# Performance work log

Hardware: AMD Instinct MI355X
Metric: run time of the kernel (lower is better)

## Reference

```python
import jax, jax.numpy as jnp
import numpy as np

B, T, H, W = 1024, 10, 32, 32
D = H * W          # MoE token dim = image_width**2
HID = 2 * D        # MoE expert hidden size
E, K = 4, 1        # num_experts, top_k
N_MOE = 5          # transform, add, quad, cubic, fourth


def setup_inputs() -> dict:
    key = jax.random.key(0)
    ks = jax.random.split(key, 6)
    s = 0.02
    return {
        "input": jax.random.normal(ks[0], (B, T, 1, H, W), jnp.float32),
        "conv1_w": jax.random.normal(ks[1], (10, 1, 3, 3, 3), jnp.float32) * s,
        "conv1_b": jnp.zeros((10,), jnp.float32),
        "conv2_w": jax.random.normal(ks[2], (1, 10, T, 3, 3), jnp.float32) * s,
        "conv2_b": jnp.zeros((1,), jnp.float32),
        "w_gate": jax.random.normal(ks[3], (N_MOE, D, E), jnp.float32) * s,
        "w1": jax.random.normal(ks[4], (N_MOE, E, D, HID), jnp.float32) * s,
        "b1": jnp.zeros((N_MOE, E, HID), jnp.float32),
        "w2": jax.random.normal(ks[5], (N_MOE, E, HID, D), jnp.float32) * s,
        "b2": jnp.zeros((N_MOE, E, D), jnp.float32),
    }


def _conv3d(x, w, b, pad):
    y = jax.lax.conv_general_dilated(
        x, w, (1, 1, 1), pad, dimension_numbers=("NCDHW", "OIDHW", "NCDHW"))
    return y + b[None, :, None, None, None]


def _cv_squared(x):
    eps = 1e-10
    return jnp.var(x, ddof=1) / (jnp.mean(x) ** 2 + eps)


def _moe(tok, wg, w1, b1, w2, b2):
    # tok: (B, D). Eval-mode noisy-top-k gating (clean logits, no noise).
    logits = tok @ wg                                   # (B, E)
    top_vals, top_idx = jax.lax.top_k(logits, K)
    top_g = jax.nn.softmax(top_vals, axis=1)            # k=1 -> gate == 1.0
    gates = jnp.zeros_like(logits).at[
        jnp.arange(tok.shape[0])[:, None], top_idx].set(top_g)
    # dense all-expert MLP (E=4 is small), combined by sparse gates
    h = jax.nn.relu(jnp.einsum("bd,edh->beh", tok, w1) + b1)
    y = jnp.einsum("beh,ehd->bed", h, w2) + b2
    out = jnp.einsum("be,bed->bd", gates, y)
    importance = gates.sum(0)
    load = (gates > 0).astype(tok.dtype).sum(0)
    loss = (_cv_squared(importance) + _cv_squared(load)) * 1e-2
    return out, loss


def reference(input, conv1_w, conv1_b, conv2_w, conv2_b, w_gate, w1, b1, w2, b2):
    x = jnp.transpose(input, (0, 2, 1, 3, 4))           # (B,1,T,H,W)
    x = jax.nn.relu(_conv3d(x, conv1_w, conv1_b, [(1, 1), (1, 1), (1, 1)]))
    x = jax.nn.relu(_conv3d(x, conv2_w, conv2_b, [(0, 0), (1, 1), (1, 1)]))  # (B,1,1,H,W)
    tok = x.reshape(x.shape[0], -1)                     # (B, D)
    outs, losses = jax.vmap(_moe, in_axes=(None, 0, 0, 0, 0, 0))(
        tok, w_gate, w1, b1, w2, b2)                    # (5,B,D), (5,)
    f = outs.reshape(N_MOE, -1, 1, 1, H, W)             # each broadcasts over T
    transform, add, quad, cubic, fourth = f[0], f[1], f[2], f[3], f[4]
    i2 = input * input
    poly = (i2 * i2 * fourth + i2 * input * cubic + i2 * quad
            + input * transform + add)
    out = jax.nn.sigmoid(poly)                          # encoder/decoder = identity
    return out, jnp.sum(losses)
```

## Files before the change

### kernel.cpp

```cpp
#include <hip/hip_runtime.h>
#include <hip/hip_bf16.h>


typedef __bf16 bf16x8 __attribute__((ext_vector_type(8)));
typedef __bf16 bf16x4 __attribute__((ext_vector_type(4)));
typedef __bf16 bf16x2 __attribute__((ext_vector_type(2)));
typedef float f32x4 __attribute__((ext_vector_type(4)));

#define NMOE 5
#define NEXP 4

__global__ __launch_bounds__(256, 3) void conv_tok_kernel(
    const float* __restrict__ input, const float* __restrict__ c1w,
    const float* __restrict__ c1b, const float* __restrict__ c2w,
    const float* __restrict__ c2b, float* __restrict__ tok_f32,
    __bf16* __restrict__ tok_bf16)
{
    __shared__ float in_s[10][34][34];
    __shared__ float P[34][34];
    const int b = blockIdx.x, tid = threadIdx.x;

    float* ls = &in_s[0][0][0];
    for (int i = tid; i < 10 * 34 * 34; i += 256) ls[i] = 0.f;
    for (int i = tid; i < 34 * 34; i += 256) (&P[0][0])[i] = 0.f;
    __syncthreads();

    const float* ip = input + (size_t)b * 10240;
    for (int i = tid; i < 2560; i += 256) {
        int t = i >> 8, rem = i & 255;
        int h = rem >> 3, w4 = rem & 7;
        float4 v = ((const float4*)ip)[i];
        float* dst = &in_s[t][h + 1][w4 * 4 + 1];
        dst[0] = v.x; dst[1] = v.y; dst[2] = v.z; dst[3] = v.w;
    }
    __syncthreads();

    const int wcol = tid & 31;
    const int r0 = (tid >> 5) * 4;
    const float c2bias = c2b[0];
    float tk0 = c2bias, tk1 = c2bias, tk2 = c2bias, tk3 = c2bias;

    for (int c = 0; c < 10; ++c) {
        float w1l[27];
        #pragma unroll
        for (int i = 0; i < 27; ++i) w1l[i] = c1w[c * 27 + i];
        const float c1bias = c1b[c];

        float a0[10], a1[10], a2[10], a3[10];
        #pragma unroll
        for (int t = 0; t < 10; ++t) {
            a0[t] = c1bias; a1[t] = c1bias; a2[t] = c1bias; a3[t] = c1bias;
        }

        #pragma unroll
        for (int ts = 0; ts < 10; ++ts) {
            float p0[3], p1[3], p2[3], p3[3], p4[3], p5[3];
            #pragma unroll
            for (int dw = 0; dw < 3; ++dw) {
                p0[dw] = in_s[ts][r0 + 0][wcol + dw];
                p1[dw] = in_s[ts][r0 + 1][wcol + dw];
                p2[dw] = in_s[ts][r0 + 2][wcol + dw];
                p3[dw] = in_s[ts][r0 + 3][wcol + dw];
                p4[dw] = in_s[ts][r0 + 4][wcol + dw];
                p5[dw] = in_s[ts][r0 + 5][wcol + dw];
            }
            #pragma unroll
            for (int dt = 0; dt < 3; ++dt) {
                const int t = ts - dt + 1;
                if (t < 0 || t > 9) continue;
                #pragma unroll
                for (int dw = 0; dw < 3; ++dw) {
                    float u0 = w1l[dt * 9 + 0 + dw];
                    float u1 = w1l[dt * 9 + 3 + dw];
                    float u2 = w1l[dt * 9 + 6 + dw];
                    a0[t] += u0 * p0[dw] + u1 * p1[dw] + u2 * p2[dw];
                    a1[t] += u0 * p1[dw] + u1 * p2[dw] + u2 * p3[dw];
                    a2[t] += u0 * p2[dw] + u1 * p3[dw] + u2 * p4[dw];
                    a3[t] += u0 * p3[dw] + u1 * p4[dw] + u2 * p5[dw];
                }
            }
            if (ts >= 1) {
                const int td = ts - 1;
                __syncthreads();
                P[r0 + 1][wcol + 1] = fmaxf(a0[td], 0.f);
                P[r0 + 2][wcol + 1] = fmaxf(a1[td], 0.f);
                P[r0 + 3][wcol + 1] = fmaxf(a2[td], 0.f);
                P[r0 + 4][wcol + 1] = fmaxf(a3[td], 0.f);
                __syncthreads();
                const int wb = (c * 10 + td) * 9;
                #pragma unroll
                for (int dw = 0; dw < 3; ++dw) {
                    float q0 = P[r0 + 0][wcol + dw];
                    float q1 = P[r0 + 1][wcol + dw];
                    float q2 = P[r0 + 2][wcol + dw];
                    float q3 = P[r0 + 3][wcol + dw];
                    float q4 = P[r0 + 4][wcol + dw];
                    float q5 = P[r0 + 5][wcol + dw];
                    float u0 = c2w[wb + 0 + dw];
                    float u1 = c2w[wb + 3 + dw];
                    float u2 = c2w[wb + 6 + dw];
                    tk0 += u0 * q0 + u1 * q1 + u2 * q2;
                    tk1 += u0 * q1 + u1 * q2 + u2 * q3;
                    tk2 += u0 * q2 + u1 * q3 + u2 * q4;
                    tk3 += u0 * q3 + u1 * q4 + u2 * q5;
                }
            }
        }
        {
            __syncthreads();
            P[r0 + 1][wcol + 1] = fmaxf(a0[9], 0.f);
            P[r0 + 2][wcol + 1] = fmaxf(a1[9], 0.f);
            P[r0 + 3][wcol + 1] = fmaxf(a2[9], 0.f);
            P[r0 + 4][wcol + 1] = fmaxf(a3[9], 0.f);
            __syncthreads();
            const int wb = (c * 10 + 9) * 9;
            #pragma unroll
            for (int dw = 0; dw < 3; ++dw) {
                float q0 = P[r0 + 0][wcol + dw];
                float q1 = P[r0 + 1][wcol + dw];
                float q2 = P[r0 + 2][wcol + dw];
                float q3 = P[r0 + 3][wcol + dw];
                float q4 = P[r0 + 4][wcol + dw];
                float q5 = P[r0 + 5][wcol + dw];
                float u0 = c2w[wb + 0 + dw];
                float u1 = c2w[wb + 3 + dw];
                float u2 = c2w[wb + 6 + dw];
                tk0 += u0 * q0 + u1 * q1 + u2 * q2;
                tk1 += u0 * q1 + u1 * q2 + u2 * q3;
                tk2 += u0 * q2 + u1 * q3 + u2 * q4;
                tk3 += u0 * q3 + u1 * q4 + u2 * q5;
            }
        }
    }
    float o0 = fmaxf(tk0, 0.f), o1 = fmaxf(tk1, 0.f);
    float o2 = fmaxf(tk2, 0.f), o3 = fmaxf(tk3, 0.f);
    size_t base = (size_t)b * 1024 + (size_t)r0 * 32 + wcol;
    tok_f32[base] = o0; tok_f32[base + 32] = o1;
    tok_f32[base + 64] = o2; tok_f32[base + 96] = o3;
    tok_bf16[base] = (__bf16)o0; tok_bf16[base + 32] = (__bf16)o1;
    tok_bf16[base + 64] = (__bf16)o2; tok_bf16[base + 96] = (__bf16)o3;
}

__global__ __launch_bounds__(256) void gating_kernel(
    const float* __restrict__ tok, const float* __restrict__ w_gate,
    int* __restrict__ expert_id, int* __restrict__ counts)
{
    int gw = blockIdx.x * 4 + (threadIdx.x >> 6);
    int l = threadIdx.x & 63;
    int n = gw >> 10, b = gw & 1023;
    const float* trow = tok + (size_t)b * 1024;
    const float* wg = w_gate + (size_t)n * 4096;
    float a0 = 0.f, a1 = 0.f, a2 = 0.f, a3 = 0.f;
    #pragma unroll
    for (int i = 0; i < 16; ++i) {
        int d = i * 64 + l;
        float tv = trow[d];
        float4 g4 = *(const float4*)(wg + d * 4);
        a0 += tv * g4.x; a1 += tv * g4.y; a2 += tv * g4.z; a3 += tv * g4.w;
    }
    #pragma unroll
    for (int off = 32; off >= 1; off >>= 1) {
        a0 += __shfl_xor(a0, off);
        a1 += __shfl_xor(a1, off);
        a2 += __shfl_xor(a2, off);
        a3 += __shfl_xor(a3, off);
    }
    if (l == 0) {
        int e = 0; float best = a0;
        if (a1 > best) { best = a1; e = 1; }
        if (a2 > best) { best = a2; e = 2; }
        if (a3 > best) { best = a3; e = 3; }
        expert_id[n * 1024 + b] = e;
        atomicAdd(&counts[n * 4 + e], 1);
    }
}

__global__ __launch_bounds__(1024) void scatter_kernel(
    const int* __restrict__ expert_id, const int* __restrict__ counts,
    int* __restrict__ row_base, int* __restrict__ rows)
{
    __shared__ int cur[4];
    int n = blockIdx.x, tid = threadIdx.x;
    if (tid == 0) {
        int c0 = counts[n * 4 + 0], c1 = counts[n * 4 + 1], c2 = counts[n * 4 + 2];
        cur[0] = 0; cur[1] = c0; cur[2] = c0 + c1; cur[3] = c0 + c1 + c2;
        row_base[n * 4 + 0] = cur[0]; row_base[n * 4 + 1] = cur[1];
        row_base[n * 4 + 2] = cur[2]; row_base[n * 4 + 3] = cur[3];
    }
    __syncthreads();
    int e = expert_id[n * 1024 + tid];
    int pos = atomicAdd(&cur[e], 1);
    rows[n * 1024 + pos] = tid;
}

template <int K, int N, int BN, bool GATHER, bool RELU, bool OUTBF>
__global__ __launch_bounds__(512) void moe_gemm_kernel(
    const __bf16* __restrict__ Abase, const float* __restrict__ Bsrc,
    const float* __restrict__ bias, const int* __restrict__ rows_all,
    const int* __restrict__ counts_all, const int* __restrict__ rowbase_all,
    __bf16* __restrict__ outB, float* __restrict__ outF)
{
    constexpr int CQ  = BN / 4;
    constexpr int UB  = BN / 64;
    constexpr int NFR = BN / 32;

    const int gy = blockIdx.y;
    const int mod = gy >> 4, rem = gy & 15;
    const int e = rem >> 2, mt = rem & 3;
    const int grp = mod * 4 + e;
    const int cnt = counts_all[grp];
    const int row0 = mt * 256;
    if (row0 >= cnt) return;
    const int rbase = rowbase_all[grp];
    const int valid = min(256, cnt - row0);
    const int n0 = blockIdx.x * BN;
    const int* rows = rows_all + mod * 1024;

    __shared__ alignas(16) __bf16 As[256 * 64];
    __shared__ alignas(16) __bf16 Bs[BN * 64];

    const int tid = threadIdx.x;
    const int l = tid & 63, w = tid >> 6;
    const int wr = w >> 1, wc = w & 1;

    const __bf16* aptr[4];
    int woffA[4];
    const __bf16* abase2 = GATHER ? Abase : (Abase + (size_t)mod * 1024 * (size_t)K);
    #pragma unroll
    for (int i = 0; i < 4; ++i) {
        int flat = tid + i * 512;
        int rr = flat >> 3, cc = flat & 7;
        int ri = rbase + row0 + min(rr, valid - 1);
        int ga = GATHER ? rows[ri] : ri;
        aptr[i] = abase2 + (size_t)ga * K + cc * 8;
        woffA[i] = rr * 64 + ((cc ^ (rr & 7)) * 8);
    }
    const float* bp0 = Bsrc + (size_t)grp * K * N + n0;
    const float* bptr[UB][2];
    int boff[UB], bx[UB];
    #pragma unroll
    for (int i = 0; i < UB; ++i) {
        int u = tid + i * 512;
        int rp = u / CQ, cq = u % CQ;
        bptr[i][0] = bp0 + (size_t)(2 * rp) * N + 4 * cq;
        bptr[i][1] = bp0 + (size_t)(2 * rp + 1) * N + 4 * cq;
        boff[i] = (4 * cq) * 64 + ((rp & 3) << 1);
        bx[i] = (rp >> 2) ^ (4 * (cq & 1)) ^ ((cq >> 1) & 7);
    }

    f32x4 acc[4][NFR];
    f32x4 zero = {0.f, 0.f, 0.f, 0.f};
    #pragma unroll
    for (int mi = 0; mi < 4; ++mi)
        #pragma unroll
        for (int ni = 0; ni < NFR; ++ni) acc[mi][ni] = zero;

    bf16x8 av[4], avn[4];
    f32x4 bv[UB][2], bvn[UB][2];
    #pragma unroll
    for (int i = 0; i < 4; ++i) av[i] = *(const bf16x8*)aptr[i];
    #pragma unroll
    for (int i = 0; i < UB; ++i) {
        bv[i][0] = *(const f32x4*)bptr[i][0];
        bv[i][1] = *(const f32x4*)bptr[i][1];
    }

    for (int k0 = 0; k0 < K; k0 += 64) {
        __syncthreads();
        #pragma unroll
        for (int i = 0; i < 4; ++i) *(bf16x8*)(As + woffA[i]) = av[i];
        #pragma unroll
        for (int i = 0; i < UB; ++i) {
            #pragma unroll
            for (int qq = 0; qq < 4; ++qq) {
                bf16x2 val = {(__bf16)bv[i][0][qq], (__bf16)bv[i][1][qq]};
                *(bf16x2*)(Bs + boff[i] + qq * 64 + ((bx[i] ^ qq) << 3)) = val;
            }
        }
        if (k0 + 64 < K) {
            #pragma unroll
            for (int i = 0; i < 4; ++i) {
                aptr[i] += 64;
                avn[i] = *(const bf16x8*)aptr[i];
            }
            #pragma unroll
            for (int i = 0; i < UB; ++i) {
                bptr[i][0] += (size_t)64 * N;
                bptr[i][1] += (size_t)64 * N;
                bvn[i][0] = *(const f32x4*)bptr[i][0];
                bvn[i][1] = *(const f32x4*)bptr[i][1];
            }
        }
        __syncthreads();
        #pragma unroll
        for (int kk = 0; kk < 2; ++kk) {
            bf16x8 af[4], bfv[NFR];
            #pragma unroll
            for (int mi = 0; mi < 4; ++mi) {
                int row = wr * 64 + mi * 16 + (l & 15);
                int cc = (kk * 4 + (l >> 4)) ^ (row & 7);
                af[mi] = *(const bf16x8*)(As + row * 64 + cc * 8);
            }
            #pragma unroll
            for (int ni = 0; ni < NFR; ++ni) {
                int nrow = wc * (BN / 2) + ni * 16 + (l & 15);
                int gg = (nrow ^ (nrow >> 3)) & 7;
                int cc = (kk * 4 + (l >> 4)) ^ gg;
                bfv[ni] = *(const bf16x8*)(Bs + nrow * 64 + cc * 8);
            }
            #pragma unroll
            for (int mi = 0; mi < 4; ++mi)
                #pragma unroll
                for (int ni = 0; ni < NFR; ++ni)
                    acc[mi][ni] = __builtin_amdgcn_mfma_f32_16x16x32_bf16(
                        af[mi], bfv[ni], acc[mi][ni], 0, 0, 0);
        }
        #pragma unroll
        for (int i = 0; i < 4; ++i) av[i] = avn[i];
        #pragma unroll
        for (int i = 0; i < UB; ++i) {
            bv[i][0] = bvn[i][0];
            bv[i][1] = bvn[i][1];
        }
    }

    const int lrow = l >> 4, lcol = l & 15;
    #pragma unroll
    for (int ni = 0; ni < NFR; ++ni) {
        int col = n0 + wc * (BN / 2) + ni * 16 + lcol;
        float bval = bias[(size_t)grp * N + col];
        #pragma unroll
        for (int mi = 0; mi < 4; ++mi) {
            #pragma unroll
            for (int j = 0; j < 4; ++j) {
                int rt = wr * 64 + mi * 16 + lrow * 4 + j;
                if (rt < valid) {
                    float v = acc[mi][ni][j] + bval;
                    if (RELU) v = fmaxf(v, 0.f);
                    int crow = rbase + row0 + rt;
                    if (OUTBF) {
                        outB[((size_t)mod * 1024 + crow) * N + col] = (__bf16)v;
                    } else {
                        int tokid = rows[crow];
                        outF[((size_t)mod * 1024 + tokid) * N + col] = v;
                    }
                }
            }
        }
    }
}

__global__ __launch_bounds__(256) void poly_kernel(
    const float* __restrict__ input, const float* __restrict__ moe,
    const int* __restrict__ counts, float* __restrict__ out,
    float* __restrict__ out_loss)
{
    const int b = blockIdx.x, tid = threadIdx.x;
    float4 f0 = *(const float4*)(moe + (size_t)(0 * 1024 + b) * 1024 + tid * 4);
    float4 f1 = *(const float4*)(moe + (size_t)(1 * 1024 + b) * 1024 + tid * 4);
    float4 f2 = *(const float4*)(moe + (size_t)(2 * 1024 + b) * 1024 + tid * 4);
    float4 f3 = *(const float4*)(moe + (size_t)(3 * 1024 + b) * 1024 + tid * 4);
    float4 f4 = *(const float4*)(moe + (size_t)(4 * 1024 + b) * 1024 + tid * 4);
    const float4* ipv = (const float4*)(input + (size_t)b * 10240);
    float4* opv = (float4*)(out + (size_t)b * 10240);
    #pragma unroll
    for (int t = 0; t < 10; ++t) {
        float4 x = ipv[t * 256 + tid];
        float4 r;
        {
            float i2 = x.x * x.x;
            float p = i2 * (i2 * f4.x + x.x * f3.x + f2.x) + x.x * f0.x + f1.x;
            r.x = 1.f / (1.f + __expf(-p));
        }
        {
            float i2 = x.y * x.y;
            float p = i2 * (i2 * f4.y + x.y * f3.y + f2.y) + x.y * f0.y + f1.y;
            r.y = 1.f / (1.f + __expf(-p));
        }
        {
            float i2 = x.z * x.z;
            float p = i2 * (i2 * f4.z + x.z * f3.z + f2.z) + x.z * f0.z + f1.z;
            r.z = 1.f / (1.f + __expf(-p));
        }
        {
            float i2 = x.w * x.w;
            float p = i2 * (i2 * f4.w + x.w * f3.w + f2.w) + x.w * f0.w + f1.w;
            r.w = 1.f / (1.f + __expf(-p));
        }
        opv[t * 256 + tid] = r;
    }
    if (b == 0 && tid == 0) {
        float total = 0.f;
        for (int n = 0; n < NMOE; ++n) {
            const float m = 256.f;
            float var = 0.f;
            for (int e = 0; e < 4; ++e) {
                float d = (float)counts[n * 4 + e] - m;
                var += d * d;
            }
            var *= (1.f / 3.f);
            float cv2 = var / (m * m + 1e-10f);
            total += 2.f * cv2 * 1e-2f;
        }
        *out_loss = total;
    }
}

extern "C" void kernel_launch(void* const* d_in, const int* in_sizes, int n_in,
                              void* d_out, int out_size, void* d_ws, size_t ws_size,
                              hipStream_t stream)
{
    (void)in_sizes; (void)n_in; (void)out_size; (void)ws_size;
    const float* input = (const float*)d_in[0];
    const float* c1w   = (const float*)d_in[1];
    const float* c1b   = (const float*)d_in[2];
    const float* c2w   = (const float*)d_in[3];
    const float* c2b   = (const float*)d_in[4];
    const float* wgate = (const float*)d_in[5];
    const float* w1    = (const float*)d_in[6];
    const float* b1    = (const float*)d_in[7];
    const float* w2    = (const float*)d_in[8];
    const float* b2    = (const float*)d_in[9];
    float* out = (float*)d_out;

    char* ws = (char*)d_ws;
    float*  tok_f32   = (float*)(ws + 0);
    __bf16* tok_bf16  = (__bf16*)(ws + 4194304);
    __bf16* h         = (__bf16*)(ws + 6291456);
    float*  moe_out   = (float*)(ws + 27262976);
    int*    rows      = (int*)(ws + 48234496);
    int*    expert_id = (int*)(ws + 48254976);
    int*    counts    = (int*)(ws + 48275456);
    int*    row_base  = (int*)(ws + 48275536);

    hipMemsetAsync(counts, 0, NMOE * NEXP * sizeof(int), stream);

    conv_tok_kernel<<<1024, 256, 0, stream>>>(input, c1w, c1b, c2w, c2b, tok_f32, tok_bf16);
    gating_kernel<<<1280, 256, 0, stream>>>(tok_f32, wgate, expert_id, counts);
    scatter_kernel<<<5, 1024, 0, stream>>>(expert_id, counts, row_base, rows);

    moe_gemm_kernel<1024, 2048, 128, true, true, true><<<dim3(16, 80), 512, 0, stream>>>(
        tok_bf16, w1, b1, rows, counts, row_base, h, nullptr);
    moe_gemm_kernel<2048, 1024, 64, false, false, false><<<dim3(16, 80), 512, 0, stream>>>(
        h, w2, b2, rows, counts, row_base, nullptr, moe_out);

    poly_kernel<<<1024, 256, 0, stream>>>(input, moe_out, counts, out, out + 10485760);
}
```

Before: 445.1 us.

## Fuse gating into conv kernel and shrink first MoE GEMM tile width

The gating dot-products are moved into the tail of the conv kernel, which reuses the freshly computed token row from LDS. This removes the fp32 token buffer write, the separate gating launch and the re-read of tokens from global memory. The first expert GEMM also switches to a 64-wide N tile with twice as many blocks along N, trading more parallelism for less per-block reuse. The conv kernel now does extra serial work per block (5 gate projections over 4 waves, so one wave does two) and reads w_gate from every block.

```diff
diff --git a/kernel.cpp b/kernel.cpp
--- a/kernel.cpp
+++ b/kernel.cpp
@@ -13,8 +13,9 @@
 __global__ __launch_bounds__(256, 3) void conv_tok_kernel(
     const float* __restrict__ input, const float* __restrict__ c1w,
     const float* __restrict__ c1b, const float* __restrict__ c2w,
-    const float* __restrict__ c2b, float* __restrict__ tok_f32,
-    __bf16* __restrict__ tok_bf16)
+    const float* __restrict__ c2b, const float* __restrict__ w_gate,
+    __bf16* __restrict__ tok_bf16, int* __restrict__ expert_id,
+    int* __restrict__ counts)
 {
     __shared__ float in_s[10][34][34];
     __shared__ float P[34][34];
@@ -135,43 +136,43 @@
     float o0 = fmaxf(tk0, 0.f), o1 = fmaxf(tk1, 0.f);
     float o2 = fmaxf(tk2, 0.f), o3 = fmaxf(tk3, 0.f);
     size_t base = (size_t)b * 1024 + (size_t)r0 * 32 + wcol;
-    tok_f32[base] = o0; tok_f32[base + 32] = o1;
-    tok_f32[base + 64] = o2; tok_f32[base + 96] = o3;
     tok_bf16[base] = (__bf16)o0; tok_bf16[base + 32] = (__bf16)o1;
     tok_bf16[base + 64] = (__bf16)o2; tok_bf16[base + 96] = (__bf16)o3;
-}
-
-__global__ __launch_bounds__(256) void gating_kernel(
-    const float* __restrict__ tok, const float* __restrict__ w_gate,
-    int* __restrict__ expert_id, int* __restrict__ counts)
-{
-    int gw = blockIdx.x * 4 + (threadIdx.x >> 6);
-    int l = threadIdx.x & 63;
-    int n = gw >> 10, b = gw & 1023;
-    const float* trow = tok + (size_t)b * 1024;
-    const float* wg = w_gate + (size_t)n * 4096;
-    float a0 = 0.f, a1 = 0.f, a2 = 0.f, a3 = 0.f;
-    #pragma unroll
-    for (int i = 0; i < 16; ++i) {
-        int d = i * 64 + l;
-        float tv = trow[d];
-        float4 g4 = *(const float4*)(wg + d * 4);
-        a0 += tv * g4.x; a1 += tv * g4.y; a2 += tv * g4.z; a3 += tv * g4.w;
-    }
-    #pragma unroll
-    for (int off = 32; off >= 1; off >>= 1) {
-        a0 += __shfl_xor(a0, off);
-        a1 += __shfl_xor(a1, off);
-        a2 += __shfl_xor(a2, off);
-        a3 += __shfl_xor(a3, off);
-    }
-    if (l == 0) {
-        int e = 0; float best = a0;
-        if (a1 > best) { best = a1; e = 1; }
-        if (a2 > best) { best = a2; e = 2; }
-        if (a3 > best) { best = a3; e = 3; }
-        expert_id[n * 1024 + b] = e;
-        atomicAdd(&counts[n * 4 + e], 1);
+
+    __syncthreads();
+    float* tokLDS = &P[0][0];
+    tokLDS[(r0 + 0) * 32 + wcol] = o0;
+    tokLDS[(r0 + 1) * 32 + wcol] = o1;
+    tokLDS[(r0 + 2) * 32 + wcol] = o2;
+    tokLDS[(r0 + 3) * 32 + wcol] = o3;
+    __syncthreads();
+
+    const int l = tid & 63, w = tid >> 6;
+    for (int n = w; n < NMOE; n += 4) {
+        const float* wg = w_gate + (size_t)n * 4096;
+        float a0 = 0.f, a1 = 0.f, a2 = 0.f, a3 = 0.f;
+        #pragma unroll
+        for (int i = 0; i < 16; ++i) {
+            int d = i * 64 + l;
+            float tv = tokLDS[d];
+            float4 g4 = *(const float4*)(wg + d * 4);
+            a0 += tv * g4.x; a1 += tv * g4.y; a2 += tv * g4.z; a3 += tv * g4.w;
+        }
+        #pragma unroll
+        for (int off = 32; off >= 1; off >>= 1) {
+            a0 += __shfl_xor(a0, off);
+            a1 += __shfl_xor(a1, off);
+            a2 += __shfl_xor(a2, off);
+            a3 += __shfl_xor(a3, off);
+        }
+        if (l == 0) {
+            int e = 0; float best = a0;
+            if (a1 > best) { best = a1; e = 1; }
+            if (a2 > best) { best = a2; e = 2; }
+            if (a3 > best) { best = a3; e = 3; }
+            expert_id[n * 1024 + b] = e;
+            atomicAdd(&counts[n * 4 + e], 1);
+        }
     }
 }
 
@@ -424,7 +425,6 @@
     float* out = (float*)d_out;
 
     char* ws = (char*)d_ws;
-    float*  tok_f32   = (float*)(ws + 0);
     __bf16* tok_bf16  = (__bf16*)(ws + 4194304);
     __bf16* h         = (__bf16*)(ws + 6291456);
     float*  moe_out   = (float*)(ws + 27262976);
@@ -435,11 +435,11 @@
 
     hipMemsetAsync(counts, 0, NMOE * NEXP * sizeof(int), stream);
 
-    conv_tok_kernel<<<1024, 256, 0, stream>>>(input, c1w, c1b, c2w, c2b, tok_f32, tok_bf16);
-    gating_kernel<<<1280, 256, 0, stream>>>(tok_f32, wgate, expert_id, counts);
+    conv_tok_kernel<<<1024, 256, 0, stream>>>(input, c1w, c1b, c2w, c2b, wgate,
+                                              tok_bf16, expert_id, counts);
     scatter_kernel<<<5, 1024, 0, stream>>>(expert_id, counts, row_base, rows);
 
-    moe_gemm_kernel<1024, 2048, 128, true, true, true><<<dim3(16, 80), 512, 0, stream>>>(
+    moe_gemm_kernel<1024, 2048, 64, true, true, true><<<dim3(32, 80), 512, 0, stream>>>(
         tok_bf16, w1, b1, rows, counts, row_base, h, nullptr);
     moe_gemm_kernel<2048, 1024, 64, false, false, false><<<dim3(16, 80), 512, 0, stream>>>(
         h, w2, b2, rows, counts, row_base, nullptr, moe_out);
```

Result: faster. 398.6 us (median of 3 runs) (-10.5%).
